# Performance work log

Hardware: AMD Instinct MI355X
Metric: run time of the kernel (lower is better)

Reference implementation:

```python
import jax, jax.numpy as jnp
import numpy as np

EPS = 1e-5  # torch InstanceNorm2d default eps

def instance_norm(x):
    # per-sample, per-channel normalization over spatial dims (affine=False)
    m = jnp.mean(x, axis=(2, 3), keepdims=True)
    v = jnp.var(x, axis=(2, 3), keepdims=True)
    return (x - m) * jax.lax.rsqrt(v + EPS)

def conv2d(x, w, b, stride, pad):
    y = jax.lax.conv_general_dilated(
        x, w, (stride, stride), [(pad, pad), (pad, pad)],
        dimension_numbers=('NCHW', 'OIHW', 'NCHW'))
    return y + b[None, :, None, None]

def res_block(x, w1, b1, w2, b2):
    out = conv2d(jax.nn.relu(instance_norm(x)), w1, b1, 1, 1)
    out = conv2d(jax.nn.relu(instance_norm(out)), w2, b2, 1, 1)
    return out + x

def res_block_strided(x, w1, b1, w2, b2, ws, bs):
    out = conv2d(jax.nn.relu(instance_norm(x)), w1, b1, 2, 1)
    out = conv2d(jax.nn.relu(instance_norm(out)), w2, b2, 1, 1)
    return out + conv2d(x, ws, bs, 2, 0)  # 1x1 strided skip projection

def setup_inputs() -> dict:
    key = jax.random.key(0)
    ks = jax.random.split(key, 12)
    B, N, C, H, W = 64, 1, 3, 256, 256
    TEXT, EMB, F, HEADS = 256, 512, 32, 5
    FH, FW = H // 16, W // 16  # 16, 16
    def rn(k, shape, scale=0.05):
        return jax.random.normal(k, shape, dtype=jnp.float32) * scale
    z = lambda *s: jnp.zeros(s, jnp.float32)
    return {
        'x': jax.random.normal(ks[0], (B, N, C, H, W), jnp.float32),
        'text_vector': jax.random.normal(ks[1], (B, TEXT), jnp.float32),
        'conv1_w': rn(ks[2], (F, C, 7, 7)),
        'conv1_b': z(F),
        'rbs_w1': rn(ks[3], (3, F, F, 3, 3)),  # 3 strided resblocks
        'rbs_b1': z(3, F),
        'rbs_w2': rn(ks[4], (3, F, F, 3, 3)),
        'rbs_b2': z(3, F),
        'rbs_ws': rn(ks[5], (3, F, F, 1, 1)),
        'rbs_bs': z(3, F),
        'rb_w1': rn(ks[6], (2, F, F, 3, 3)),  # 2 plain resblocks
        'rb_b1': z(2, F),
        'rb_w2': rn(ks[7], (2, F, F, 3, 3)),
        'rb_b2': z(2, F),
        'attn_w': rn(ks[8], (HEADS, FH * FW, TEXT)),  # torch Linear [out,in] per head
        'attn_b': z(HEADS, FH * FW),
        'final_w': rn(ks[9], (EMB, FH * FW * HEADS)),
        'final_b': z(EMB),
    }

def reference(x, text_vector, conv1_w, conv1_b, rbs_w1, rbs_b1, rbs_w2, rbs_b2,
              rbs_ws, rbs_bs, rb_w1, rb_b1, rb_w2, rb_b2, attn_w, attn_b,
              final_w, final_b):
    B, N, C, H, W = x.shape
    feat = x.reshape(B, N * C, H, W)
    feat = instance_norm(feat)
    feat = conv2d(feat, conv1_w, conv1_b, 2, 3)
    # block1 = strided + plain; block2 = strided + plain; block3 = strided
    feat = res_block_strided(feat, rbs_w1[0], rbs_b1[0], rbs_w2[0], rbs_b2[0], rbs_ws[0], rbs_bs[0])
    feat = res_block(feat, rb_w1[0], rb_b1[0], rb_w2[0], rb_b2[0])
    feat = res_block_strided(feat, rbs_w1[1], rbs_b1[1], rbs_w2[1], rbs_b2[1], rbs_ws[1], rbs_bs[1])
    feat = res_block(feat, rb_w1[1], rb_b1[1], rb_w2[1], rb_b2[1])
    feat = res_block_strided(feat, rbs_w1[2], rbs_b1[2], rbs_w2[2], rbs_b2[2], rbs_ws[2], rbs_bs[2])
    # feat: [B, 32, FH, FW]
    HEADS = attn_w.shape[0]
    FH, FW = feat.shape[2], feat.shape[3]
    # sigmoid-gated spatial attention logits per head: [B, HEADS, FH, FW]
    a = jax.nn.sigmoid(jnp.einsum('bt,hot->bho', text_vector, attn_w) + attn_b[None])
    a = a.reshape(B, HEADS, FH, FW)
    # channel scores: spatial sum of gate * feature -> [B, HEADS, C]
    scores = jnp.einsum('bhij,bcij->bhc', a, feat)
    probs = jax.nn.softmax(scores, axis=-1)  # old F.softmax over channel dim
    # weighted channel sum -> per-head attention map [B, HEADS, FH, FW]
    amaps = jnp.einsum('bhc,bcij->bhij', probs, feat)
    out = amaps.reshape(B, -1) @ final_w.T + final_b
    return out
```

## Files before the change

kernel.cpp:

```cpp
#include <hip/hip_runtime.h>
#include <cstdint>
#include <cstddef>

#define INORM_EPS 1e-5f

typedef _Float16 f16;
typedef f16 f16x8 __attribute__((ext_vector_type(8)));
typedef f16 f16x4 __attribute__((ext_vector_type(4)));
typedef float f32x4 __attribute__((ext_vector_type(4)));

__global__ __launch_bounds__(256) void prep_stats(
    const float* __restrict__ rbs_w1, const float* __restrict__ rbs_w2,
    const float* __restrict__ rb_w1, const float* __restrict__ rb_w2,
    const float* __restrict__ rbs_ws, const float* __restrict__ conv1_w,
    const float* __restrict__ x, float2* __restrict__ SP,
    f16* __restrict__ wp3, f16* __restrict__ wp1, f16* __restrict__ wp7,
    float2* __restrict__ SPx8) {
  const int bx = blockIdx.x;
  if (bx >= 480) {
    const int g = bx - 480;
    const int map = g >> 3, chunk = g & 7;
    const float4* p = (const float4*)(x + (size_t)map * 65536 + (size_t)chunk * 8192);
    float s = 0.f, ss = 0.f;
    for (int i = threadIdx.x; i < 2048; i += 256) {
      float4 v = p[i];
      s += v.x + v.y + v.z + v.w;
      ss += v.x * v.x + v.y * v.y + v.z * v.z + v.w * v.w;
    }
    __shared__ float r0[256], r1[256];
    r0[threadIdx.x] = s;
    r1[threadIdx.x] = ss;
    __syncthreads();
    for (int off = 128; off > 0; off >>= 1) {
      if ((int)threadIdx.x < off) {
        r0[threadIdx.x] += r0[threadIdx.x + off];
        r1[threadIdx.x] += r1[threadIdx.x + off];
      }
      __syncthreads();
    }
    if (threadIdx.x == 0) SPx8[map * 8 + chunk] = make_float2(r0[0], r1[0]);
    return;
  }
  int i = bx * 256 + threadIdx.x;
  if (i < 20480) { SP[i] = make_float2(0.f, 0.f); return; }
  i -= 20480;
  if (i < 92160) {
    int mat = i / 9216, r = i % 9216;
    int p = r >> 10, f = (r >> 9) & 1, l = (r >> 3) & 63, j = r & 7;
    int co = f * 16 + (l & 15), ci = (l >> 4) * 8 + j;
    const float* src; int m;
    if (mat < 3) { src = rbs_w1; m = mat; }
    else if (mat < 6) { src = rbs_w2; m = mat - 3; }
    else if (mat < 8) { src = rb_w1; m = mat - 6; }
    else { src = rb_w2; m = mat - 8; }
    wp3[i] = (f16)src[m * 9216 + co * 288 + ci * 9 + p];
    return;
  }
  i -= 92160;
  if (i < 3072) {
    int mat = i / 1024, r = i % 1024;
    int f = r >> 9, l = (r >> 3) & 63, j = r & 7;
    wp1[i] = (f16)rbs_ws[mat * 1024 + (f * 16 + (l & 15)) * 32 + (l >> 4) * 8 + j];
    return;
  }
  i -= 3072;
  if (i >= 7168) return;
  int ky = i >> 10, f = (i >> 9) & 1, l = (i >> 3) & 63, j = i & 7;
  int k = (l >> 4) * 8 + j, kx = k >> 2, ci = k & 3;
  float v = 0.f;
  if (kx < 7 && ci < 3) v = conv1_w[(f * 16 + (l & 15)) * 147 + ci * 49 + ky * 7 + kx];
  wp7[i] = (f16)v;
}

template <int W, int SKIP, int RPB>
__global__ __launch_bounds__(256) void conv3r(
    const f16* __restrict__ Rin, const float2* __restrict__ SPin, float inv_hw,
    const f16* __restrict__ wp, const float* __restrict__ bias,
    const float* __restrict__ bias2, const f16* __restrict__ skip,
    const f16* __restrict__ wps, f16* __restrict__ Rout,
    float2* __restrict__ ostats) {
  constexpr int TPR = W / 16;
  constexpr int LEN = (RPB * TPR) / 4;
  const int t = threadIdx.x, w = t >> 6, l = t & 63;
  const int n = l & 15, q = l >> 4;
  const int b = blockIdx.z;
  const int tx = w % TPR;
  const int y0 = blockIdx.x * RPB + (w / TPR) * LEN;
  const int x = (tx << 4) + n;
  const f16* Rb = Rin + (size_t)b * W * W * 32;

  f16x8 sc, sh;
#pragma unroll
  for (int j = 0; j < 8; j++) {
    float2 s = SPin[b * 32 + q * 8 + j];
    float mean = s.x * inv_hw;
    float rstd = rsqrtf(s.y * inv_hw - mean * mean + INORM_EPS);
    sc[j] = (f16)rstd;
    sh[j] = (f16)(-mean * rstd);
  }

  f16x8 wf[18];
#pragma unroll
  for (int i = 0; i < 18; i++) wf[i] = *(const f16x8*)(wp + i * 512 + l * 8);
  f16x8 wsf0, wsf1;
  if (SKIP == 2) {
    wsf0 = *(const f16x8*)(wps + l * 8);
    wsf1 = *(const f16x8*)(wps + 512 + l * 8);
  }
  float b0 = bias[n], b1 = bias[16 + n];
  if (SKIP == 2) { b0 += bias2[n]; b1 += bias2[16 + n]; }

  f16* ro = Rout + (size_t)b * W * W * 32;
  const f16* sb = skip ? skip + (size_t)b * (SKIP == 2 ? 4 : 1) * W * W * 32 : nullptr;

  bool okc[3];
#pragma unroll
  for (int kx = 0; kx < 3; kx++) okc[kx] = (unsigned)(x + kx - 1) < (unsigned)W;

  auto rowload = [&](int gy, f16x8* dst) {
    int gyc = min(max(gy, 0), W - 1);
#pragma unroll
    for (int kx = 0; kx < 3; kx++) {
      int gxc = min(max(x + kx - 1, 0), W - 1);
      dst[kx] = *(const f16x8*)(Rb + ((size_t)gyc * W + gxc) * 32 + q * 8);
    }
  };
  auto rownorm = [&](int gy, const f16x8* src, f16x8* dst) {
    bool okr = (unsigned)gy < (unsigned)W;
#pragma unroll
    for (int kx = 0; kx < 3; kx++) {
      f16x8 v = src[kx] * sc + sh;
#pragma unroll
      for (int e = 0; e < 8; e++) v[e] = v[e] > (f16)0 ? v[e] : (f16)0;
      f16x8 z = {};
      dst[kx] = (okr && okc[kx]) ? v : z;
    }
  };

  float sm0 = 0.f, sq0 = 0.f, sm1 = 0.f, sq1 = 0.f;
  f16x8 win[9];
  f16x8 pf[3][3];
#pragma unroll
  for (int jj = 0; jj < 3; jj++) rowload(y0 + jj - 1, &win[jj * 3]);
  if (LEN > 1) rowload(y0 + 2, pf[0]);
  if (LEN > 2) rowload(y0 + 3, pf[1]);
#pragma unroll
  for (int jj = 0; jj < 3; jj++) rownorm(y0 + jj - 1, &win[jj * 3], &win[jj * 3]);

#pragma unroll
  for (int i = 0; i < LEN; i++) {
    int y = y0 + i;
    if (i + 3 < LEN) rowload(y0 + i + 4, pf[(i + 2) % 3]);
    f32x4 acc0 = {0.f, 0.f, 0.f, 0.f}, acc1 = {0.f, 0.f, 0.f, 0.f};
#pragma unroll
    for (int ky = 0; ky < 3; ky++) {
      int slot = (i + ky) % 3;
#pragma unroll
      for (int kx = 0; kx < 3; kx++) {
        f16x8 a = win[slot * 3 + kx];
        acc0 = __builtin_amdgcn_mfma_f32_16x16x32_f16(a, wf[2 * (ky * 3 + kx)], acc0, 0, 0, 0);
        acc1 = __builtin_amdgcn_mfma_f32_16x16x32_f16(a, wf[2 * (ky * 3 + kx) + 1], acc1, 0, 0, 0);
      }
    }
    if (SKIP == 2) {
      const int Ws = 2 * W;
      f16x8 as = *(const f16x8*)(sb + ((size_t)(2 * y) * Ws + 2 * x) * 32 + q * 8);
      acc0 = __builtin_amdgcn_mfma_f32_16x16x32_f16(as, wsf0, acc0, 0, 0, 0);
      acc1 = __builtin_amdgcn_mfma_f32_16x16x32_f16(as, wsf1, acc1, 0, 0, 0);
    }
#pragma unroll
    for (int r = 0; r < 4; r++) {
      size_t px = (size_t)y * W + (tx << 4) + q * 4 + r;
      float v0 = acc0[r] + b0;
      float v1 = acc1[r] + b1;
      if (SKIP == 1) {
        v0 += (float)sb[px * 32 + n];
        v1 += (float)sb[px * 32 + 16 + n];
      }
      ro[px * 32 + n] = (f16)v0;
      ro[px * 32 + 16 + n] = (f16)v1;
      sm0 += v0; sq0 += v0 * v0;
      sm1 += v1; sq1 += v1 * v1;
    }
    if (i + 1 < LEN) rownorm(y0 + i + 2, pf[i % 3], &win[(i % 3) * 3]);
  }
  if (ostats) {
    sm0 += __shfl_xor(sm0, 16); sm0 += __shfl_xor(sm0, 32);
    sq0 += __shfl_xor(sq0, 16); sq0 += __shfl_xor(sq0, 32);
    sm1 += __shfl_xor(sm1, 16); sm1 += __shfl_xor(sm1, 32);
    sq1 += __shfl_xor(sq1, 16); sq1 += __shfl_xor(sq1, 32);
    if (l < 16) {
      atomicAdd(&ostats[b * 32 + n].x, sm0);
      atomicAdd(&ostats[b * 32 + n].y, sq0);
      atomicAdd(&ostats[b * 32 + 16 + n].x, sm1);
      atomicAdd(&ostats[b * 32 + 16 + n].y, sq1);
    }
  }
}

template <int WIN>
__global__ __launch_bounds__(256) void conv3s2(
    const f16* __restrict__ Rin, const float2* __restrict__ SPin, float inv_hw,
    const f16* __restrict__ wp, const float* __restrict__ bias,
    f16* __restrict__ Rout, float2* __restrict__ ostats) {
  constexpr int WOUT = WIN / 2;
  constexpr int TPR = WOUT / 16;
  constexpr int RPB = 8;
  constexpr int LEN = (RPB * TPR) / 4;
  const int t = threadIdx.x, w = t >> 6, l = t & 63;
  const int n = l & 15, q = l >> 4;
  const int b = blockIdx.z;
  const int tx = w % TPR;
  const int y0 = blockIdx.x * RPB + (w / TPR) * LEN;
  const int x = (tx << 4) + n;
  const f16* Rb = Rin + (size_t)b * WIN * WIN * 32;

  f16x8 sc, sh;
#pragma unroll
  for (int j = 0; j < 8; j++) {
    float2 s = SPin[b * 32 + q * 8 + j];
    float mean = s.x * inv_hw;
    float rstd = rsqrtf(s.y * inv_hw - mean * mean + INORM_EPS);
    sc[j] = (f16)rstd;
    sh[j] = (f16)(-mean * rstd);
  }

  f16x8 wf[18];
#pragma unroll
  for (int i = 0; i < 18; i++) wf[i] = *(const f16x8*)(wp + i * 512 + l * 8);
  float b0 = bias[n], b1 = bias[16 + n];

  f16* ro = Rout + (size_t)b * WOUT * WOUT * 32;

  bool okc[3];
#pragma unroll
  for (int kx = 0; kx < 3; kx++) okc[kx] = (unsigned)(2 * x + kx - 1) < (unsigned)WIN;

  auto rowload = [&](int gy, f16x8* dst) {
    int gyc = min(max(gy, 0), WIN - 1);
#pragma unroll
    for (int kx = 0; kx < 3; kx++) {
      int gxc = min(max(2 * x + kx - 1, 0), WIN - 1);
      dst[kx] = *(const f16x8*)(Rb + ((size_t)gyc * WIN + gxc) * 32 + q * 8);
    }
  };
  auto rownorm = [&](int gy, const f16x8* src, f16x8* dst) {
    bool okr = (unsigned)gy < (unsigned)WIN;
#pragma unroll
    for (int kx = 0; kx < 3; kx++) {
      f16x8 v = src[kx] * sc + sh;
#pragma unroll
      for (int e = 0; e < 8; e++) v[e] = v[e] > (f16)0 ? v[e] : (f16)0;
      f16x8 z = {};
      dst[kx] = (okr && okc[kx]) ? v : z;
    }
  };

  float sm0 = 0.f, sq0 = 0.f, sm1 = 0.f, sq1 = 0.f;
  f16x8 win[9], pa[3], pb[3];
#pragma unroll
  for (int jj = 0; jj < 3; jj++) {
    rowload(2 * y0 - 1 + jj, pa);
    rownorm(2 * y0 - 1 + jj, pa, &win[jj * 3]);
  }

#pragma unroll
  for (int i = 0; i < LEN; i++) {
    int y = y0 + i;
    if (i + 1 < LEN) {
      rowload(2 * y + 2, pa);
      rowload(2 * y + 3, pb);
    }
    f32x4 acc0 = {0.f, 0.f, 0.f, 0.f}, acc1 = {0.f, 0.f, 0.f, 0.f};
#pragma unroll
    for (int ky = 0; ky < 3; ky++) {
      int slot = (2 * i + ky) % 3;
#pragma unroll
      for (int kx = 0; kx < 3; kx++) {
        f16x8 a = win[slot * 3 + kx];
        acc0 = __builtin_amdgcn_mfma_f32_16x16x32_f16(a, wf[2 * (ky * 3 + kx)], acc0, 0, 0, 0);
        acc1 = __builtin_amdgcn_mfma_f32_16x16x32_f16(a, wf[2 * (ky * 3 + kx) + 1], acc1, 0, 0, 0);
      }
    }
#pragma unroll
    for (int r = 0; r < 4; r++) {
      size_t px = (size_t)y * WOUT + (tx << 4) + q * 4 + r;
      float v0 = acc0[r] + b0;
      float v1 = acc1[r] + b1;
      ro[px * 32 + n] = (f16)v0;
      ro[px * 32 + 16 + n] = (f16)v1;
      sm0 += v0; sq0 += v0 * v0;
      sm1 += v1; sq1 += v1 * v1;
    }
    if (i + 1 < LEN) {
      rownorm(2 * y + 2, pa, &win[((2 * i + 3) % 3) * 3]);
      rownorm(2 * y + 3, pb, &win[((2 * i + 4) % 3) * 3]);
    }
  }
  if (ostats) {
    sm0 += __shfl_xor(sm0, 16); sm0 += __shfl_xor(sm0, 32);
    sq0 += __shfl_xor(sq0, 16); sq0 += __shfl_xor(sq0, 32);
    sm1 += __shfl_xor(sm1, 16); sm1 += __shfl_xor(sm1, 32);
    sq1 += __shfl_xor(sq1, 16); sq1 += __shfl_xor(sq1, 32);
    if (l < 16) {
      atomicAdd(&ostats[b * 32 + n].x, sm0);
      atomicAdd(&ostats[b * 32 + n].y, sq0);
      atomicAdd(&ostats[b * 32 + 16 + n].x, sm1);
      atomicAdd(&ostats[b * 32 + 16 + n].y, sq1);
    }
  }
}

template <int WIN, int STRIDE, int SKIP, int RPB>
__global__ __launch_bounds__(256) void conv3n(
    const f16* __restrict__ Rin, const float2* __restrict__ SPin, float inv_hw,
    const f16* __restrict__ wp, const float* __restrict__ bias,
    const float* __restrict__ bias2, const f16* __restrict__ skip,
    const f16* __restrict__ wps, f16* __restrict__ Rout,
    float2* __restrict__ ostats) {
  constexpr int WOUT = WIN / STRIDE;
  constexpr int TPR = WOUT / 16;
  constexpr int UNITS = TPR * RPB;
  constexpr int U = UNITS / 4;
  static_assert(U >= 1, "need at least one unit per wave");
  constexpr int NB = (U >= 3) ? 3 : ((U >= 2) ? 2 : 1);
  const int t = threadIdx.x, w = t >> 6, l = t & 63;
  const int n = l & 15, q = l >> 4;
  const int b = blockIdx.z;
  const int yb = blockIdx.x * RPB;
  const f16* Rb = Rin + (size_t)b * WIN * WIN * 32;

  f16x8 sc, sh;
#pragma unroll
  for (int j = 0; j < 8; j++) {
    float2 s = SPin[b * 32 + q * 8 + j];
    float mean = s.x * inv_hw;
    float rstd = rsqrtf(s.y * inv_hw - mean * mean + INORM_EPS);
    sc[j] = (f16)rstd;
    sh[j] = (f16)(-mean * rstd);
  }

  f16x8 wf[18];
#pragma unroll
  for (int i = 0; i < 18; i++) wf[i] = *(const f16x8*)(wp + i * 512 + l * 8);
  f16x8 wsf0, wsf1;
  if (SKIP == 2) {
    wsf0 = *(const f16x8*)(wps + l * 8);
    wsf1 = *(const f16x8*)(wps + 512 + l * 8);
  }
  float b0 = bias[n], b1 = bias[16 + n];
  if (SKIP == 2) { b0 += bias2[n]; b1 += bias2[16 + n]; }

  f16* ro = Rout + (size_t)b * WOUT * WOUT * 32;
  const f16* sb = skip ? skip + (size_t)b * (SKIP == 2 ? 4 : 1) * WOUT * WOUT * 32 : nullptr;

  auto load_u = [&](int u, f16x8* a) {
    int ty = u / TPR, tx = u % TPR;
    int y = yb + ty;
#pragma unroll
    for (int kx = 0; kx < 3; kx++) {
      int gx = STRIDE * ((tx << 4) + n) + kx - 1;
      int gxc = min(max(gx, 0), WIN - 1);
#pragma unroll
      for (int ky = 0; ky < 3; ky++) {
        int gy = STRIDE * y + ky - 1;
        int gyc = min(max(gy, 0), WIN - 1);
        a[ky * 3 + kx] = *(const f16x8*)(Rb + ((size_t)gyc * WIN + gxc) * 32 + q * 8);
      }
    }
  };
  auto norm_u = [&](int u, f16x8* a) {
    int ty = u / TPR, tx = u % TPR;
    int y = yb + ty;
#pragma unroll
    for (int kx = 0; kx < 3; kx++) {
      int gx = STRIDE * ((tx << 4) + n) + kx - 1;
      bool okx = (unsigned)gx < (unsigned)WIN;
#pragma unroll
      for (int ky = 0; ky < 3; ky++) {
        int gy = STRIDE * y + ky - 1;
        bool ok = okx && ((unsigned)gy < (unsigned)WIN);
        f16x8 v = a[ky * 3 + kx] * sc + sh;
#pragma unroll
        for (int e = 0; e < 8; e++) v[e] = v[e] > (f16)0 ? v[e] : (f16)0;
        f16x8 z = {};
        a[ky * 3 + kx] = ok ? v : z;
      }
    }
  };

  float sm0 = 0.f, sq0 = 0.f, sm1 = 0.f, sq1 = 0.f;
  f16x8 buf[NB][9];
  load_u(w, buf[0]);
  if (U > 1) load_u(w + 4, buf[1 % NB]);
#pragma unroll
  for (int i = 0; i < U; i++) {
    int u = w + 4 * i;
    if (i + 2 < U) load_u(u + 8, buf[(i + 2) % NB]);
    f16x8* a = buf[i % NB];
    norm_u(u, a);
    int ty = u / TPR, tx = u % TPR;
    int y = yb + ty, x0 = tx << 4;
    f32x4 acc0 = {0.f, 0.f, 0.f, 0.f}, acc1 = {0.f, 0.f, 0.f, 0.f};
#pragma unroll
    for (int p = 0; p < 9; p++) {
      acc0 = __builtin_amdgcn_mfma_f32_16x16x32_f16(a[p], wf[2 * p], acc0, 0, 0, 0);
      acc1 = __builtin_amdgcn_mfma_f32_16x16x32_f16(a[p], wf[2 * p + 1], acc1, 0, 0, 0);
    }
    if (SKIP == 2) {
      const int Ws = 2 * WOUT;
      f16x8 as = *(const f16x8*)(sb + ((size_t)(2 * y) * Ws + 2 * (x0 + n)) * 32 + q * 8);
      acc0 = __builtin_amdgcn_mfma_f32_16x16x32_f16(as, wsf0, acc0, 0, 0, 0);
      acc1 = __builtin_amdgcn_mfma_f32_16x16x32_f16(as, wsf1, acc1, 0, 0, 0);
    }
#pragma unroll
    for (int r = 0; r < 4; r++) {
      size_t px = (size_t)y * WOUT + x0 + q * 4 + r;
      float v0 = acc0[r] + b0;
      float v1 = acc1[r] + b1;
      if (SKIP == 1) {
        v0 += (float)sb[px * 32 + n];
        v1 += (float)sb[px * 32 + 16 + n];
      }
      ro[px * 32 + n] = (f16)v0;
      ro[px * 32 + 16 + n] = (f16)v1;
      sm0 += v0; sq0 += v0 * v0;
      sm1 += v1; sq1 += v1 * v1;
    }
  }
  if (ostats) {
    sm0 += __shfl_xor(sm0, 16); sm0 += __shfl_xor(sm0, 32);
    sq0 += __shfl_xor(sq0, 16); sq0 += __shfl_xor(sq0, 32);
    sm1 += __shfl_xor(sm1, 16); sm1 += __shfl_xor(sm1, 32);
    sq1 += __shfl_xor(sq1, 16); sq1 += __shfl_xor(sq1, 32);
    if (l < 16) {
      atomicAdd(&ostats[b * 32 + n].x, sm0);
      atomicAdd(&ostats[b * 32 + n].y, sq0);
      atomicAdd(&ostats[b * 32 + 16 + n].x, sm1);
      atomicAdd(&ostats[b * 32 + 16 + n].y, sq1);
    }
  }
}

__global__ __launch_bounds__(256) void conv7(
    const float* __restrict__ x, const float2* __restrict__ SPx8,
    const f16* __restrict__ wp, const float* __restrict__ bias,
    f16* __restrict__ Rout, float2* __restrict__ ostats) {
  __shared__ f16 lds[21 * 131 * 8];
  const int t = threadIdx.x, w = t >> 6, l = t & 63;
  const int n = l & 15, q = l >> 4;
  const int b = blockIdx.z;
  const int yb = blockIdx.x * 8;
  const float* Xb = x + (size_t)b * 3 * 65536;
  float mn[3], rs[3];
#pragma unroll
  for (int ci = 0; ci < 3; ci++) {
    float sx = 0.f, sxx = 0.f;
#pragma unroll
    for (int c = 0; c < 8; c++) {
      float2 v = SPx8[(b * 3 + ci) * 8 + c];
      sx += v.x; sxx += v.y;
    }
    mn[ci] = sx * (1.f / 65536.f);
    rs[ci] = rsqrtf(sxx * (1.f / 65536.f) - mn[ci] * mn[ci] + INORM_EPS);
  }
  f16x8 wf[14];
#pragma unroll
  for (int i = 0; i < 14; i++) wf[i] = *(const f16x8*)(wp + i * 512 + l * 8);
  float b0 = bias[n], b1 = bias[16 + n];

  for (int idx = t; idx < 7 * 262; idx += 256) {
    int ri = idx / 262, cl = idx - ri * 262;
    int row = 2 * yb - 3 + ri, col = cl - 3;
    bool ok = ((unsigned)row < 256u) && ((unsigned)col < 256u);
    f16x4 v = {};
    if (ok) {
      const float* p = Xb + (size_t)row * 256 + col;
      v[0] = (f16)((p[0] - mn[0]) * rs[0]);
      v[1] = (f16)((p[65536] - mn[1]) * rs[1]);
      v[2] = (f16)((p[131072] - mn[2]) * rs[2]);
    }
    *(f16x4*)(lds + ((ri * 131 + (cl >> 1)) * 8) + (cl & 1) * 4) = v;
  }
  __syncthreads();

  float sm0 = 0.f, sq0 = 0.f, sm1 = 0.f, sq1 = 0.f;
  f16* ro = Rout + (size_t)b * 16384 * 32;

  auto compute_chunk = [&](int i0, int i1) {
#pragma unroll
    for (int seg = 0; seg < 2; seg++) {
      const int tx = w + seg * 4;
      const int x0 = tx * 16;
      const int u = x0 + n + q;
      for (int i = i0; i < i1; i++) {
        int y = yb + i;
        f32x4 acc0 = {0.f, 0.f, 0.f, 0.f}, acc1 = {0.f, 0.f, 0.f, 0.f};
#pragma unroll
        for (int ky = 0; ky < 7; ky++) {
          f16x8 a = *(const f16x8*)(lds + ((2 * i + ky) * 131 + u) * 8);
          acc0 = __builtin_amdgcn_mfma_f32_16x16x32_f16(a, wf[2 * ky], acc0, 0, 0, 0);
          acc1 = __builtin_amdgcn_mfma_f32_16x16x32_f16(a, wf[2 * ky + 1], acc1, 0, 0, 0);
        }
#pragma unroll
        for (int r = 0; r < 4; r++) {
          size_t px = (size_t)y * 128 + x0 + q * 4 + r;
          float v0 = acc0[r] + b0;
          float v1 = acc1[r] + b1;
          ro[px * 32 + n] = (f16)v0;
          ro[px * 32 + 16 + n] = (f16)v1;
          sm0 += v0; sq0 += v0 * v0;
          sm1 += v1; sq1 += v1 * v1;
        }
      }
    }
  };

  float ub0[7], ub1[7], ub2[7];
#pragma unroll
  for (int it = 0; it < 7; it++) {
    int idx = t + it * 256;
    int ri = idx / 262, cl = idx - ri * 262;
    int row = 2 * yb + 4 + ri, col = cl - 3;
    bool ok = (idx < 1572) && (row < 256) && ((unsigned)col < 256u);
    const float* p = Xb + (size_t)(ok ? row : 0) * 256 + (ok ? col : 0);
    ub0[it] = p[0];
    ub1[it] = p[65536];
    ub2[it] = p[131072];
  }

  compute_chunk(0, 1);

#pragma unroll
  for (int it = 0; it < 7; it++) {
    int idx = t + it * 256;
    if (idx < 1572) {
      int ri = idx / 262, cl = idx - ri * 262;
      int row = 2 * yb + 4 + ri, col = cl - 3;
      bool ok = (row < 256) && ((unsigned)col < 256u);
      f16x4 v = {};
      if (ok) {
        v[0] = (f16)((ub0[it] - mn[0]) * rs[0]);
        v[1] = (f16)((ub1[it] - mn[1]) * rs[1]);
        v[2] = (f16)((ub2[it] - mn[2]) * rs[2]);
      }
      *(f16x4*)(lds + (((7 + ri) * 131 + (cl >> 1)) * 8) + (cl & 1) * 4) = v;
    }
  }

  float uc0[7], uc1[7], uc2[7];
#pragma unroll
  for (int it = 0; it < 7; it++) {
    int idx = t + it * 256;
    int ri = idx / 262, cl = idx - ri * 262;
    int row = 2 * yb + 10 + ri, col = cl - 3;
    bool ok = (idx < 1572) && (row < 256) && ((unsigned)col < 256u);
    const float* p = Xb + (size_t)(ok ? row : 0) * 256 + (ok ? col : 0);
    uc0[it] = p[0];
    uc1[it] = p[65536];
    uc2[it] = p[131072];
  }
  __syncthreads();

  compute_chunk(1, 4);

#pragma unroll
  for (int it = 0; it < 7; it++) {
    int idx = t + it * 256;
    if (idx < 1572) {
      int ri = idx / 262, cl = idx - ri * 262;
      int row = 2 * yb + 10 + ri, col = cl - 3;
      bool ok = (row < 256) && ((unsigned)col < 256u);
      f16x4 v = {};
      if (ok) {
        v[0] = (f16)((uc0[it] - mn[0]) * rs[0]);
        v[1] = (f16)((uc1[it] - mn[1]) * rs[1]);
        v[2] = (f16)((uc2[it] - mn[2]) * rs[2]);
      }
      *(f16x4*)(lds + (((13 + ri) * 131 + (cl >> 1)) * 8) + (cl & 1) * 4) = v;
    }
  }

  float ud0[3], ud1[3], ud2[3];
#pragma unroll
  for (int it = 0; it < 3; it++) {
    int idx = t + it * 256;
    int ri = idx / 262, cl = idx - ri * 262;
    int row = 2 * yb + 16 + ri, col = cl - 3;
    bool ok = (idx < 524) && (row < 256) && ((unsigned)col < 256u);
    const float* p = Xb + (size_t)(ok ? row : 0) * 256 + (ok ? col : 0);
    ud0[it] = p[0];
    ud1[it] = p[65536];
    ud2[it] = p[131072];
  }
  __syncthreads();

  compute_chunk(4, 7);

#pragma unroll
  for (int it = 0; it < 3; it++) {
    int idx = t + it * 256;
    if (idx < 524) {
      int ri = idx / 262, cl = idx - ri * 262;
      int row = 2 * yb + 16 + ri, col = cl - 3;
      bool ok = (row < 256) && ((unsigned)col < 256u);
      f16x4 v = {};
      if (ok) {
        v[0] = (f16)((ud0[it] - mn[0]) * rs[0]);
        v[1] = (f16)((ud1[it] - mn[1]) * rs[1]);
        v[2] = (f16)((ud2[it] - mn[2]) * rs[2]);
      }
      *(f16x4*)(lds + (((19 + ri) * 131 + (cl >> 1)) * 8) + (cl & 1) * 4) = v;
    }
  }
  __syncthreads();

  compute_chunk(7, 8);

  sm0 += __shfl_xor(sm0, 16); sm0 += __shfl_xor(sm0, 32);
  sq0 += __shfl_xor(sq0, 16); sq0 += __shfl_xor(sq0, 32);
  sm1 += __shfl_xor(sm1, 16); sm1 += __shfl_xor(sm1, 32);
  sq1 += __shfl_xor(sq1, 16); sq1 += __shfl_xor(sq1, 32);
  if (l < 16) {
    atomicAdd(&ostats[b * 32 + n].x, sm0);
    atomicAdd(&ostats[b * 32 + n].y, sq0);
    atomicAdd(&ostats[b * 32 + 16 + n].x, sm1);
    atomicAdd(&ostats[b * 32 + 16 + n].y, sq1);
  }
}

__global__ __launch_bounds__(256) void gates_kernel(
    const float* __restrict__ text, const float* __restrict__ attn_w,
    const float* __restrict__ attn_b, float* __restrict__ G) {
  __shared__ float s_text[64 * 257];
  __shared__ float s_w[16 * 256];
  const int t = threadIdx.x, wv = t >> 6, lane = t & 63;
  const int o0 = blockIdx.x * 16;
  for (int d = t; d < 16384; d += 256) {
    int b = d >> 8, k = d & 255;
    s_text[b * 257 + k] = text[d];
  }
  for (int d = t; d < 4096; d += 256) s_w[d] = attn_w[(size_t)o0 * 256 + d];
  __syncthreads();
  float acc[4];
#pragma unroll
  for (int j = 0; j < 4; j++) acc[j] = attn_b[o0 + wv * 4 + j];
  for (int k = 0; k < 256; k++) {
    float tv = s_text[lane * 257 + k];
#pragma unroll
    for (int j = 0; j < 4; j++) acc[j] = fmaf(s_w[(wv * 4 + j) * 256 + k], tv, acc[j]);
  }
#pragma unroll
  for (int j = 0; j < 4; j++) {
    int o = o0 + wv * 4 + j;
    G[o * 64 + lane] = 1.f / (1.f + __expf(-acc[j]));
  }
}

__global__ __launch_bounds__(256) void scores_kernel(
    const f16* __restrict__ feat, const float* __restrict__ G,
    float* __restrict__ amapT) {
  __shared__ float s_feat[256 * 33];
  __shared__ float s_gate[1280];
  __shared__ float s_scores[5 * 32];
  __shared__ float s_probs[5 * 32];
  const int b = blockIdx.x;
  const int t = threadIdx.x;

  for (int i = t; i < 8192; i += 256)
    s_feat[(i >> 5) * 33 + (i & 31)] = (float)feat[(size_t)b * 8192 + i];
  for (int i = t; i < 1280; i += 256) s_gate[i] = G[i * 64 + b];
  __syncthreads();

  if (t < 160) {
    int h = t >> 5, c = t & 31;
    float acc = 0.f;
    for (int ij = 0; ij < 256; ij++) acc += s_gate[h * 256 + ij] * s_feat[ij * 33 + c];
    s_scores[t] = acc;
  }
  __syncthreads();

  if (t < 5) {
    float mx = -1e30f;
    for (int c = 0; c < 32; c++) mx = fmaxf(mx, s_scores[t * 32 + c]);
    float sum = 0.f;
    for (int c = 0; c < 32; c++) {
      float e = __expf(s_scores[t * 32 + c] - mx);
      s_probs[t * 32 + c] = e;
      sum += e;
    }
    float inv = 1.f / sum;
    for (int c = 0; c < 32; c++) s_probs[t * 32 + c] *= inv;
  }
  __syncthreads();

  for (int h = 0; h < 5; h++) {
    float acc = 0.f;
    for (int c = 0; c < 32; c++) acc += s_probs[h * 32 + c] * s_feat[t * 33 + c];
    amapT[(h * 256 + t) * 64 + b] = acc;
  }
}

__global__ __launch_bounds__(256) void final_kernel(
    const float* __restrict__ amapT, const float* __restrict__ final_w,
    const float* __restrict__ final_b, float* __restrict__ out) {
  __shared__ float s_w[4 * 1280];
  __shared__ float s_red[4][4][64];
  const int t = threadIdx.x, wv = t >> 6, lane = t & 63;
  const int e0 = blockIdx.x * 4;
  for (int d = t; d < 5120; d += 256) s_w[d] = final_w[(size_t)e0 * 1280 + d];
  __syncthreads();
  const int k0 = wv * 320;
  float acc[4] = {0.f, 0.f, 0.f, 0.f};
  for (int k = k0; k < k0 + 320; k++) {
    float av = amapT[k * 64 + lane];
#pragma unroll
    for (int e = 0; e < 4; e++) acc[e] = fmaf(s_w[e * 1280 + k], av, acc[e]);
  }
#pragma unroll
  for (int e = 0; e < 4; e++) s_red[wv][e][lane] = acc[e];
  __syncthreads();
  if (wv == 0) {
#pragma unroll
    for (int e = 0; e < 4; e++) {
      float v = s_red[0][e][lane] + s_red[1][e][lane] + s_red[2][e][lane] +
                s_red[3][e][lane] + final_b[e0 + e];
      out[(size_t)lane * 512 + e0 + e] = v;
    }
  }
}

extern "C" void kernel_launch(void* const* d_in, const int* in_sizes, int n_in,
                              void* d_out, int out_size, void* d_ws, size_t ws_size,
                              hipStream_t stream) {
  (void)in_sizes; (void)n_in; (void)out_size; (void)ws_size;
  const float* x       = (const float*)d_in[0];
  const float* text    = (const float*)d_in[1];
  const float* conv1_w = (const float*)d_in[2];
  const float* conv1_b = (const float*)d_in[3];
  const float* rbs_w1  = (const float*)d_in[4];
  const float* rbs_b1  = (const float*)d_in[5];
  const float* rbs_w2  = (const float*)d_in[6];
  const float* rbs_b2  = (const float*)d_in[7];
  const float* rbs_ws  = (const float*)d_in[8];
  const float* rbs_bs  = (const float*)d_in[9];
  const float* rb_w1   = (const float*)d_in[10];
  const float* rb_b1   = (const float*)d_in[11];
  const float* rb_w2   = (const float*)d_in[12];
  const float* rb_b2   = (const float*)d_in[13];
  const float* attn_w  = (const float*)d_in[14];
  const float* attn_b  = (const float*)d_in[15];
  const float* final_w = (const float*)d_in[16];
  const float* final_b = (const float*)d_in[17];
  float* out = (float*)d_out;

  char* wsb = (char*)d_ws;
  float2* SPx8 = (float2*)(wsb + 0);
  f16*   R128 = (f16*)(wsb + 35145728);
  f16*   R64a = (f16*)(wsb + 102254592);
  f16*   R64b = (f16*)(wsb + 119031808);
  f16*   R64c = (f16*)(wsb + 135809024);
  f16*   R32a = (f16*)(wsb + 152586240);
  f16*   R32b = (f16*)(wsb + 156780544);
  f16*   R32c = (f16*)(wsb + 160974848);
  f16*   R16a = (f16*)(wsb + 165169152);
  f16*   R16b = (f16*)(wsb + 166217728);
  float2* SP  = (float2*)(wsb + 167266304);
  f16*   wp3  = (f16*)(wsb + 167431680);
  f16*   wp1  = (f16*)(wsb + 167616000);
  f16*   wp7  = (f16*)(wsb + 167622144);
  float* G     = (float*)(wsb + 167636480);
  float* amapT = (float*)(wsb + 167964160);
  float2* SP0 = SP + 0 * 2048;
  float2* SP1 = SP + 1 * 2048;
  float2* SP2 = SP + 2 * 2048;
  float2* SP3 = SP + 3 * 2048;
  float2* SP4 = SP + 4 * 2048;
  float2* SP5 = SP + 5 * 2048;
  float2* SP6 = SP + 6 * 2048;
  float2* SP7 = SP + 7 * 2048;
  float2* SP8 = SP + 8 * 2048;
  float2* SP9 = SP + 9 * 2048;

  prep_stats<<<2016, 256, 0, stream>>>(rbs_w1, rbs_w2, rb_w1, rb_w2, rbs_ws,
                                       conv1_w, x, SP, wp3, wp1, wp7, SPx8);

  conv7<<<dim3(16, 1, 64), 256, 0, stream>>>(x, SPx8, wp7, conv1_b, R128, SP0);

  conv3s2<128><<<dim3(8, 1, 64), 256, 0, stream>>>(
      R128, SP0, 1.f / 16384.f, wp3, rbs_b1, R64a, SP1);
  conv3r<64, 2, 8><<<dim3(8, 1, 64), 256, 0, stream>>>(
      R64a, SP1, 1.f / 4096.f, wp3 + 3 * 9216, rbs_b2, rbs_bs, R128, wp1, R64b, SP2);

  conv3r<64, 0, 8><<<dim3(8, 1, 64), 256, 0, stream>>>(
      R64b, SP2, 1.f / 4096.f, wp3 + 6 * 9216, rb_b1, nullptr, nullptr, nullptr, R64c, SP3);
  conv3r<64, 1, 8><<<dim3(8, 1, 64), 256, 0, stream>>>(
      R64c, SP3, 1.f / 4096.f, wp3 + 8 * 9216, rb_b2, nullptr, R64b, nullptr, R64a, SP4);

  conv3s2<64><<<dim3(4, 1, 64), 256, 0, stream>>>(
      R64a, SP4, 1.f / 4096.f, wp3 + 1 * 9216, rbs_b1 + 32, R32a, SP5);
  conv3r<32, 2, 8><<<dim3(4, 1, 64), 256, 0, stream>>>(
      R32a, SP5, 1.f / 1024.f, wp3 + 4 * 9216, rbs_b2 + 32, rbs_bs + 32, R64a, wp1 + 1024, R32b, SP6);

  conv3r<32, 0, 8><<<dim3(4, 1, 64), 256, 0, stream>>>(
      R32b, SP6, 1.f / 1024.f, wp3 + 7 * 9216, rb_b1 + 32, nullptr, nullptr, nullptr, R32c, SP7);
  conv3r<32, 1, 8><<<dim3(4, 1, 64), 256, 0, stream>>>(
      R32c, SP7, 1.f / 1024.f, wp3 + 9 * 9216, rb_b2 + 32, nullptr, R32b, nullptr, R32a, SP8);

  conv3n<32, 2, 0, 8><<<dim3(2, 1, 64), 256, 0, stream>>>(
      R32a, SP8, 1.f / 1024.f, wp3 + 2 * 9216, rbs_b1 + 64, nullptr, nullptr, nullptr, R16a, SP9);
  conv3n<16, 1, 2, 8><<<dim3(2, 1, 64), 256, 0, stream>>>(
      R16a, SP9, 1.f / 256.f, wp3 + 5 * 9216, rbs_b2 + 64, rbs_bs + 64, R32a, wp1 + 2048, R16b, nullptr);

  gates_kernel<<<80, 256, 0, stream>>>(text, attn_w, attn_b, G);
  scores_kernel<<<64, 256, 0, stream>>>(R16b, G, amapT);
  final_kernel<<<128, 256, 0, stream>>>(amapT, final_w, final_b, out);
}
```

Measured before the change: 300.9 us.

## Stage conv weights in LDS, halve rows per block, raise occupancy

The 3x3 conv kernels now copy their weight fragments into shared memory once per block and read them from LDS inside the MFMA loop, instead of holding 18 f16x8 weight vectors in registers. The row-prefetch buffer shrinks from three to two rows, and launch bounds request 4 blocks per CU. Rows per block drop from 8 to 4, doubling the grid, to lower register pressure and raise occupancy and parallelism. The cost is extra LDS reads per MFMA, a block-wide barrier, and a repeated weight load across more blocks.

```diff
diff --git a/kernel.cpp b/kernel.cpp
--- a/kernel.cpp
+++ b/kernel.cpp
@@ -73,7 +73,7 @@
 }
 
 template <int W, int SKIP, int RPB>
-__global__ __launch_bounds__(256) void conv3r(
+__global__ __launch_bounds__(256, 4) void conv3r(
     const f16* __restrict__ Rin, const float2* __restrict__ SPin, float inv_hw,
     const f16* __restrict__ wp, const float* __restrict__ bias,
     const float* __restrict__ bias2, const f16* __restrict__ skip,
@@ -81,6 +81,7 @@
     float2* __restrict__ ostats) {
   constexpr int TPR = W / 16;
   constexpr int LEN = (RPB * TPR) / 4;
+  __shared__ f16 lws[9216];
   const int t = threadIdx.x, w = t >> 6, l = t & 63;
   const int n = l & 15, q = l >> 4;
   const int b = blockIdx.z;
@@ -89,6 +90,9 @@
   const int x = (tx << 4) + n;
   const f16* Rb = Rin + (size_t)b * W * W * 32;
 
+  for (int d = t; d < 2304; d += 256)
+    ((f16x4*)lws)[d] = ((const f16x4*)wp)[d];
+
   f16x8 sc, sh;
 #pragma unroll
   for (int j = 0; j < 8; j++) {
@@ -99,9 +103,6 @@
     sh[j] = (f16)(-mean * rstd);
   }
 
-  f16x8 wf[18];
-#pragma unroll
-  for (int i = 0; i < 18; i++) wf[i] = *(const f16x8*)(wp + i * 512 + l * 8);
   f16x8 wsf0, wsf1;
   if (SKIP == 2) {
     wsf0 = *(const f16x8*)(wps + l * 8);
@@ -139,18 +140,18 @@
 
   float sm0 = 0.f, sq0 = 0.f, sm1 = 0.f, sq1 = 0.f;
   f16x8 win[9];
-  f16x8 pf[3][3];
+  f16x8 pf[2][3];
 #pragma unroll
   for (int jj = 0; jj < 3; jj++) rowload(y0 + jj - 1, &win[jj * 3]);
   if (LEN > 1) rowload(y0 + 2, pf[0]);
-  if (LEN > 2) rowload(y0 + 3, pf[1]);
 #pragma unroll
   for (int jj = 0; jj < 3; jj++) rownorm(y0 + jj - 1, &win[jj * 3], &win[jj * 3]);
+  __syncthreads();
 
 #pragma unroll
   for (int i = 0; i < LEN; i++) {
     int y = y0 + i;
-    if (i + 3 < LEN) rowload(y0 + i + 4, pf[(i + 2) % 3]);
+    if (i + 2 < LEN) rowload(y0 + i + 3, pf[(i + 1) & 1]);
     f32x4 acc0 = {0.f, 0.f, 0.f, 0.f}, acc1 = {0.f, 0.f, 0.f, 0.f};
 #pragma unroll
     for (int ky = 0; ky < 3; ky++) {
@@ -158,8 +159,10 @@
 #pragma unroll
       for (int kx = 0; kx < 3; kx++) {
         f16x8 a = win[slot * 3 + kx];
-        acc0 = __builtin_amdgcn_mfma_f32_16x16x32_f16(a, wf[2 * (ky * 3 + kx)], acc0, 0, 0, 0);
-        acc1 = __builtin_amdgcn_mfma_f32_16x16x32_f16(a, wf[2 * (ky * 3 + kx) + 1], acc1, 0, 0, 0);
+        f16x8 w0 = *(const f16x8*)(lws + 2 * (ky * 3 + kx) * 512 + l * 8);
+        f16x8 w1 = *(const f16x8*)(lws + (2 * (ky * 3 + kx) + 1) * 512 + l * 8);
+        acc0 = __builtin_amdgcn_mfma_f32_16x16x32_f16(a, w0, acc0, 0, 0, 0);
+        acc1 = __builtin_amdgcn_mfma_f32_16x16x32_f16(a, w1, acc1, 0, 0, 0);
       }
     }
     if (SKIP == 2) {
@@ -182,7 +185,7 @@
       sm0 += v0; sq0 += v0 * v0;
       sm1 += v1; sq1 += v1 * v1;
     }
-    if (i + 1 < LEN) rownorm(y0 + i + 2, pf[i % 3], &win[(i % 3) * 3]);
+    if (i + 1 < LEN) rownorm(y0 + i + 2, pf[i & 1], &win[(i % 3) * 3]);
   }
   if (ostats) {
     sm0 += __shfl_xor(sm0, 16); sm0 += __shfl_xor(sm0, 32);
@@ -198,15 +201,15 @@
   }
 }
 
-template <int WIN>
-__global__ __launch_bounds__(256) void conv3s2(
+template <int WIN, int RPB>
+__global__ __launch_bounds__(256, 4) void conv3s2(
     const f16* __restrict__ Rin, const float2* __restrict__ SPin, float inv_hw,
     const f16* __restrict__ wp, const float* __restrict__ bias,
     f16* __restrict__ Rout, float2* __restrict__ ostats) {
   constexpr int WOUT = WIN / 2;
   constexpr int TPR = WOUT / 16;
-  constexpr int RPB = 8;
   constexpr int LEN = (RPB * TPR) / 4;
+  __shared__ f16 lws[9216];
   const int t = threadIdx.x, w = t >> 6, l = t & 63;
   const int n = l & 15, q = l >> 4;
   const int b = blockIdx.z;
@@ -215,6 +218,9 @@
   const int x = (tx << 4) + n;
   const f16* Rb = Rin + (size_t)b * WIN * WIN * 32;
 
+  for (int d = t; d < 2304; d += 256)
+    ((f16x4*)lws)[d] = ((const f16x4*)wp)[d];
+
   f16x8 sc, sh;
 #pragma unroll
   for (int j = 0; j < 8; j++) {
@@ -224,10 +230,6 @@
     sc[j] = (f16)rstd;
     sh[j] = (f16)(-mean * rstd);
   }
-
-  f16x8 wf[18];
-#pragma unroll
-  for (int i = 0; i < 18; i++) wf[i] = *(const f16x8*)(wp + i * 512 + l * 8);
   float b0 = bias[n], b1 = bias[16 + n];
 
   f16* ro = Rout + (size_t)b * WOUT * WOUT * 32;
@@ -263,6 +265,7 @@
     rowload(2 * y0 - 1 + jj, pa);
     rownorm(2 * y0 - 1 + jj, pa, &win[jj * 3]);
   }
+  __syncthreads();
 
 #pragma unroll
   for (int i = 0; i < LEN; i++) {
@@ -278,8 +281,10 @@
 #pragma unroll
       for (int kx = 0; kx < 3; kx++) {
         f16x8 a = win[slot * 3 + kx];
-        acc0 = __builtin_amdgcn_mfma_f32_16x16x32_f16(a, wf[2 * (ky * 3 + kx)], acc0, 0, 0, 0);
-        acc1 = __builtin_amdgcn_mfma_f32_16x16x32_f16(a, wf[2 * (ky * 3 + kx) + 1], acc1, 0, 0, 0);
+        f16x8 w0 = *(const f16x8*)(lws + 2 * (ky * 3 + kx) * 512 + l * 8);
+        f16x8 w1 = *(const f16x8*)(lws + (2 * (ky * 3 + kx) + 1) * 512 + l * 8);
+        acc0 = __builtin_amdgcn_mfma_f32_16x16x32_f16(a, w0, acc0, 0, 0, 0);
+        acc1 = __builtin_amdgcn_mfma_f32_16x16x32_f16(a, w1, acc1, 0, 0, 0);
       }
     }
 #pragma unroll
@@ -787,24 +792,24 @@
 
   conv7<<<dim3(16, 1, 64), 256, 0, stream>>>(x, SPx8, wp7, conv1_b, R128, SP0);
 
-  conv3s2<128><<<dim3(8, 1, 64), 256, 0, stream>>>(
+  conv3s2<128, 4><<<dim3(16, 1, 64), 256, 0, stream>>>(
       R128, SP0, 1.f / 16384.f, wp3, rbs_b1, R64a, SP1);
-  conv3r<64, 2, 8><<<dim3(8, 1, 64), 256, 0, stream>>>(
+  conv3r<64, 2, 4><<<dim3(16, 1, 64), 256, 0, stream>>>(
       R64a, SP1, 1.f / 4096.f, wp3 + 3 * 9216, rbs_b2, rbs_bs, R128, wp1, R64b, SP2);
 
-  conv3r<64, 0, 8><<<dim3(8, 1, 64), 256, 0, stream>>>(
+  conv3r<64, 0, 4><<<dim3(16, 1, 64), 256, 0, stream>>>(
       R64b, SP2, 1.f / 4096.f, wp3 + 6 * 9216, rb_b1, nullptr, nullptr, nullptr, R64c, SP3);
-  conv3r<64, 1, 8><<<dim3(8, 1, 64), 256, 0, stream>>>(
+  conv3r<64, 1, 4><<<dim3(16, 1, 64), 256, 0, stream>>>(
       R64c, SP3, 1.f / 4096.f, wp3 + 8 * 9216, rb_b2, nullptr, R64b, nullptr, R64a, SP4);
 
-  conv3s2<64><<<dim3(4, 1, 64), 256, 0, stream>>>(
+  conv3s2<64, 4><<<dim3(8, 1, 64), 256, 0, stream>>>(
       R64a, SP4, 1.f / 4096.f, wp3 + 1 * 9216, rbs_b1 + 32, R32a, SP5);
-  conv3r<32, 2, 8><<<dim3(4, 1, 64), 256, 0, stream>>>(
+  conv3r<32, 2, 4><<<dim3(8, 1, 64), 256, 0, stream>>>(
       R32a, SP5, 1.f / 1024.f, wp3 + 4 * 9216, rbs_b2 + 32, rbs_bs + 32, R64a, wp1 + 1024, R32b, SP6);
 
-  conv3r<32, 0, 8><<<dim3(4, 1, 64), 256, 0, stream>>>(
+  conv3r<32, 0, 4><<<dim3(8, 1, 64), 256, 0, stream>>>(
       R32b, SP6, 1.f / 1024.f, wp3 + 7 * 9216, rb_b1 + 32, nullptr, nullptr, nullptr, R32c, SP7);
-  conv3r<32, 1, 8><<<dim3(4, 1, 64), 256, 0, stream>>>(
+  conv3r<32, 1, 4><<<dim3(8, 1, 64), 256, 0, stream>>>(
       R32c, SP7, 1.f / 1024.f, wp3 + 9 * 9216, rb_b2 + 32, nullptr, R32b, nullptr, R32a, SP8);
 
   conv3n<32, 2, 0, 8><<<dim3(2, 1, 64), 256, 0, stream>>>(
```

Measured after the change: 355.0 us. 18.0% more time.
